# Kernel optimization log

Hardware: AMD Instinct MI355X
Metric: run time of the kernel (lower is better)

## Reference

```python
import jax, jax.numpy as jnp
import numpy as np

N = 100000
E = 1200000


def _gcn_norm(edge_index, num_nodes):
    # Add self-loops and compute symmetric normalization (PyG GCNConv default).
    row = jnp.concatenate([edge_index[0], jnp.arange(num_nodes, dtype=edge_index.dtype)])
    col = jnp.concatenate([edge_index[1], jnp.arange(num_nodes, dtype=edge_index.dtype)])
    deg = jax.ops.segment_sum(jnp.ones_like(col, dtype=jnp.float32), col, num_segments=num_nodes)
    dinv = jnp.where(deg > 0, jax.lax.rsqrt(jnp.maximum(deg, 1.0)), 0.0)
    norm = dinv[row] * dinv[col]  # [E+N]
    return row, col, norm


def _gcn_conv(x, W, b, row, col, norm, num_nodes):
    h = x @ W                      # [N, out] dense transform first (fewer bytes to gather)
    msg = h[row] * norm[:, None]   # gather + edge-wise scale
    out = jax.ops.segment_sum(msg, col, num_segments=num_nodes)  # scatter-add to targets
    return out + b


def setup_inputs() -> dict:
    key = jax.random.key(0)
    k1, k2, k3, k4 = jax.random.split(key, 4)
    x = jax.random.normal(k1, (N, 128), dtype=jnp.float32)
    edge_index = jax.random.randint(k2, (2, E), 0, N, dtype=jnp.int64)
    W1 = jax.random.normal(k3, (128, 256), dtype=jnp.float32) * (1.0 / np.sqrt(128))
    b1 = jnp.zeros((256,), dtype=jnp.float32)
    W2 = jax.random.normal(k4, (256, 40), dtype=jnp.float32) * (1.0 / np.sqrt(256))
    b2 = jnp.zeros((40,), dtype=jnp.float32)
    return {"x": x, "edge_index": edge_index, "W1": W1, "b1": b1, "W2": W2, "b2": b2}


def reference(x, edge_index, W1, b1, W2, b2):
    row, col, norm = _gcn_norm(edge_index, N)
    h = _gcn_conv(x, W1, b1, row, col, norm, N)
    h = jax.nn.relu(h)
    # dropout omitted: eval mode (training=False) is identity
    return _gcn_conv(h, W2, b2, row, col, norm, N)
```

## Files before the change

### kernel.cpp

```cpp
#include <hip/hip_runtime.h>
#include <hip/hip_bf16.h>

#define NN 100000
#define EE 1200000
#define F1 128
#define F2 256
#define F3 40
#define MROWS 64
#define NBUK ((NN + 255) / 256)
#define NBLK 256
#define CHUNK ((EE + NBLK - 1) / NBLK)
#define DCAP 4096
#define XB ((NN * 64 + 255) / 256)

typedef __bf16 bf16x8 __attribute__((ext_vector_type(8)));
typedef float  f32x4  __attribute__((ext_vector_type(4)));

__device__ __forceinline__ unsigned short f2bf(float f) {
    unsigned u = __float_as_uint(f);
    return (unsigned short)((u + 0x7fffu + ((u >> 16) & 1u)) >> 16);
}
__device__ __forceinline__ float bflo(unsigned v) { return __uint_as_float(v << 16); }
__device__ __forceinline__ float bfhi(unsigned v) { return __uint_as_float(v & 0xffff0000u); }

__global__ __launch_bounds__(256) void k_hist(const int* __restrict__ col,
                                              int* __restrict__ hist) {
    __shared__ int lh[NBUK];
    for (int i = threadIdx.x; i < NBUK; i += 256) lh[i] = 0;
    __syncthreads();
    int e0 = blockIdx.x * CHUNK;
    int e1 = min(e0 + CHUNK, EE);
    for (int e = e0 + threadIdx.x; e < e1; e += 256) {
        int c = col[e];
        if ((unsigned)c < (unsigned)NN) atomicAdd(&lh[c >> 8], 1);
    }
    __syncthreads();
    for (int i = threadIdx.x; i < NBUK; i += 256) hist[i * NBLK + blockIdx.x] = lh[i];
}

__global__ __launch_bounds__(256) void k_scanbin(int* __restrict__ hist,
                                                 int* __restrict__ bintot) {
    __shared__ int s[NBLK];
    int b = blockIdx.x;
    int v = hist[b * NBLK + threadIdx.x];
    s[threadIdx.x] = v;
    __syncthreads();
    int acc = v;
    for (int d = 1; d < NBLK; d <<= 1) {
        int add = (threadIdx.x >= d) ? s[threadIdx.x - d] : 0;
        __syncthreads();
        acc += add;
        s[threadIdx.x] = acc;
        __syncthreads();
    }
    hist[b * NBLK + threadIdx.x] = acc - v;
    if (threadIdx.x == NBLK - 1) bintot[b] = acc;
}

__global__ __launch_bounds__(512) void k_scanbase(const int* __restrict__ bintot,
                                                  int* __restrict__ binbase) {
    __shared__ int s[512];
    int v = (threadIdx.x < NBUK) ? bintot[threadIdx.x] : 0;
    s[threadIdx.x] = v;
    __syncthreads();
    int acc = v;
    for (int d = 1; d < 512; d <<= 1) {
        int add = (threadIdx.x >= d) ? s[threadIdx.x - d] : 0;
        __syncthreads();
        acc += add;
        s[threadIdx.x] = acc;
        __syncthreads();
    }
    if (threadIdx.x < NBUK) binbase[threadIdx.x] = acc - v;
    if (threadIdx.x == NBUK - 1) binbase[NBUK] = acc;
}

__global__ __launch_bounds__(256) void k_scat(const int* __restrict__ row,
                                              const int* __restrict__ col,
                                              const int* __restrict__ hist,
                                              const int* __restrict__ binbase,
                                              unsigned* __restrict__ rec) {
    __shared__ int lcur[NBUK];
    for (int i = threadIdx.x; i < NBUK; i += 256)
        lcur[i] = binbase[i] + hist[i * NBLK + blockIdx.x];
    __syncthreads();
    int e0 = blockIdx.x * CHUNK;
    int e1 = min(e0 + CHUNK, EE);
    for (int e = e0 + threadIdx.x; e < e1; e += 256) {
        int r = row[e], c = col[e];
        if ((unsigned)c < (unsigned)NN) {
            int pos = atomicAdd(&lcur[c >> 8], 1);
            rec[pos] = ((unsigned)r & 0xFFFFFFu) | ((unsigned)(c & 255) << 24);
        }
    }
}

__global__ __launch_bounds__(256) void k_csr(const int* __restrict__ binbase,
                                             const unsigned* __restrict__ rec,
                                             int* __restrict__ eidx,
                                             int* __restrict__ cnt,
                                             int* __restrict__ cursor,
                                             float* __restrict__ dinv) {
    __shared__ int lcnt[256];
    __shared__ int s[256];
    __shared__ int lcur[256];
    __shared__ int lde[DCAP];
    const int b = blockIdx.x;
    const int tid = threadIdx.x;
    lcnt[tid] = 0;
    __syncthreads();
    const int base = binbase[b];
    const int nb = min(binbase[b + 1] - base, DCAP);
    for (int j = tid; j < nb; j += 256) atomicAdd(&lcnt[rec[base + j] >> 24], 1);
    __syncthreads();
    int cv = lcnt[tid];
    s[tid] = cv;
    __syncthreads();
    int acc = cv;
    for (int d = 1; d < 256; d <<= 1) {
        int add = (tid >= d) ? s[tid - d] : 0;
        __syncthreads();
        acc += add;
        s[tid] = acc;
        __syncthreads();
    }
    int excl = acc - cv;
    lcur[tid] = excl;
    const int node = (b << 8) + tid;
    if (node < NN) {
        cnt[node] = cv;
        cursor[node] = base + excl + cv;
        dinv[node] = rsqrtf((float)(cv + 1));
    }
    __syncthreads();
    for (int j = tid; j < nb; j += 256) {
        unsigned v = rec[base + j];
        int pos = atomicAdd(&lcur[v >> 24], 1);
        lde[pos] = (int)(v & 0xFFFFFFu);
    }
    __syncthreads();
    for (int j = tid; j < nb; j += 256) eidx[base + j] = lde[j];
}

__global__ void k_prep(const float2* __restrict__ x, const float* __restrict__ dinv,
                       unsigned* __restrict__ xh,
                       const float* __restrict__ W1, const float* __restrict__ W2,
                       __hip_bfloat16* __restrict__ W1p, __hip_bfloat16* __restrict__ W2p) {
    if (blockIdx.x < XB) {
        int idx = blockIdx.x * 256 + threadIdx.x;
        if (idx < NN * 64) {
            float d = dinv[idx >> 6];
            float2 v = x[idx];
            xh[idx] = (unsigned)f2bf(v.x * d) | ((unsigned)f2bf(v.y * d) << 16);
        }
    } else {
        int idx = (blockIdx.x - XB) * 256 + threadIdx.x;
        if (idx < F1 * F2) {
            int k = idx / F2, col = idx - (idx / F2) * F2;
            int k8 = k >> 3, j = k & 7;
            W1p[((size_t)(k8 * F2 + col) << 3) + j] = __float2bfloat16(W1[(size_t)k * F2 + col]);
        } else if (idx < F1 * F2 + F2 * 48) {
            int i2 = idx - F1 * F2;
            int k = i2 / 48, col = i2 - (i2 / 48) * 48;
            int k8 = k >> 3, j = k & 7;
            float v = (col < F3) ? W2[(size_t)k * F3 + col] : 0.0f;
            W2p[((size_t)(k8 * 48 + col) << 3) + j] = __float2bfloat16(v);
        }
    }
}

__global__ __launch_bounds__(256) void k_agg1(const int* __restrict__ cursor,
                                              const int* __restrict__ cnt,
                                              const int* __restrict__ eidx,
                                              const float* __restrict__ dinv,
                                              const unsigned* __restrict__ xh,
                                              unsigned* __restrict__ agg) {
    int node = blockIdx.x * 4 + (threadIdx.x >> 6);
    int lane = threadIdx.x & 63;
    if (node >= NN) return;
    const int g = lane >> 4;
    const int l = lane & 15;
    float a0, a1, a2, a3, a4, a5, a6, a7;
    {
        uint4 v = {0u, 0u, 0u, 0u};
        if (g == 0) v = *(const uint4*)(xh + ((size_t)node << 6) + (l << 2));
        a0 = bflo(v.x); a1 = bfhi(v.x); a2 = bflo(v.y); a3 = bfhi(v.y);
        a4 = bflo(v.z); a5 = bfhi(v.z); a6 = bflo(v.w); a7 = bfhi(v.w);
    }
    int n = cnt[node];
    int s = cursor[node] - n;
    int k = 0;
    for (; k + 7 < n; k += 8) {
        int r0 = eidx[s + k + g];
        int r1 = eidx[s + k + 4 + g];
        uint4 v0 = *(const uint4*)(xh + ((size_t)r0 << 6) + (l << 2));
        uint4 v1 = *(const uint4*)(xh + ((size_t)r1 << 6) + (l << 2));
        a0 += bflo(v0.x); a1 += bfhi(v0.x); a2 += bflo(v0.y); a3 += bfhi(v0.y);
        a4 += bflo(v0.z); a5 += bfhi(v0.z); a6 += bflo(v0.w); a7 += bfhi(v0.w);
        a0 += bflo(v1.x); a1 += bfhi(v1.x); a2 += bflo(v1.y); a3 += bfhi(v1.y);
        a4 += bflo(v1.z); a5 += bfhi(v1.z); a6 += bflo(v1.w); a7 += bfhi(v1.w);
    }
    for (; k < n; k += 4) {
        if (k + g < n) {
            int r0 = eidx[s + k + g];
            uint4 v0 = *(const uint4*)(xh + ((size_t)r0 << 6) + (l << 2));
            a0 += bflo(v0.x); a1 += bfhi(v0.x); a2 += bflo(v0.y); a3 += bfhi(v0.y);
            a4 += bflo(v0.z); a5 += bfhi(v0.z); a6 += bflo(v0.w); a7 += bfhi(v0.w);
        }
    }
    a0 += __shfl_down(a0, 32, 64); a1 += __shfl_down(a1, 32, 64);
    a2 += __shfl_down(a2, 32, 64); a3 += __shfl_down(a3, 32, 64);
    a4 += __shfl_down(a4, 32, 64); a5 += __shfl_down(a5, 32, 64);
    a6 += __shfl_down(a6, 32, 64); a7 += __shfl_down(a7, 32, 64);
    a0 += __shfl_down(a0, 16, 64); a1 += __shfl_down(a1, 16, 64);
    a2 += __shfl_down(a2, 16, 64); a3 += __shfl_down(a3, 16, 64);
    a4 += __shfl_down(a4, 16, 64); a5 += __shfl_down(a5, 16, 64);
    a6 += __shfl_down(a6, 16, 64); a7 += __shfl_down(a7, 16, 64);
    if (g == 0) {
        float d = dinv[node];
        uint4 o;
        o.x = (unsigned)f2bf(a0 * d) | ((unsigned)f2bf(a1 * d) << 16);
        o.y = (unsigned)f2bf(a2 * d) | ((unsigned)f2bf(a3 * d) << 16);
        o.z = (unsigned)f2bf(a4 * d) | ((unsigned)f2bf(a5 * d) << 16);
        o.w = (unsigned)f2bf(a6 * d) | ((unsigned)f2bf(a7 * d) << 16);
        *(uint4*)(agg + ((size_t)node << 6) + (l << 2)) = o;
    }
}

__global__ __launch_bounds__(256) void k_gemm_mfma(
    const __hip_bfloat16* __restrict__ agg, const __hip_bfloat16* __restrict__ W1p,
    const float* __restrict__ b1, const __hip_bfloat16* __restrict__ W2p,
    const float* __restrict__ dinv, unsigned short* __restrict__ tg) {
    __shared__ __hip_bfloat16 h_s[MROWS][F2 + 8];
    const int i0   = blockIdx.x * MROWS;
    const int wave = threadIdx.x >> 6;
    const int lane = threadIdx.x & 63;
    const int m = lane & 15, q = lane >> 4;
    const int rowA = i0 + wave * 16 + m;

    f32x4 acc[16];
#pragma unroll
    for (int c = 0; c < 16; ++c) acc[c] = (f32x4){0.f, 0.f, 0.f, 0.f};

#pragma unroll
    for (int s = 0; s < 4; ++s) {
        bf16x8 a;
#pragma unroll
        for (int j = 0; j < 8; ++j) a[j] = (__bf16)0.0f;
        if (rowA < NN) a = *(const bf16x8*)(agg + (size_t)rowA * F1 + s * 32 + q * 8);
        const __hip_bfloat16* bp = W1p + ((size_t)(4 * s + q) * F2) * 8;
#pragma unroll
        for (int c = 0; c < 16; ++c) {
            bf16x8 b = *(const bf16x8*)(bp + ((size_t)(c * 16 + m) << 3));
            acc[c] = __builtin_amdgcn_mfma_f32_16x16x32_bf16(a, b, acc[c], 0, 0, 0);
        }
    }

#pragma unroll
    for (int c = 0; c < 16; ++c) {
        int col = c * 16 + m;
        float bj = b1[col];
#pragma unroll
        for (int r = 0; r < 4; ++r) {
            int lr = wave * 16 + q * 4 + r;
            h_s[lr][col] = __float2bfloat16(fmaxf(acc[c][r] + bj, 0.0f));
        }
    }
    __syncthreads();

    f32x4 acc2[3];
#pragma unroll
    for (int c = 0; c < 3; ++c) acc2[c] = (f32x4){0.f, 0.f, 0.f, 0.f};

#pragma unroll
    for (int s = 0; s < 8; ++s) {
        bf16x8 a = *(const bf16x8*)(&h_s[wave * 16 + m][s * 32 + q * 8]);
        const __hip_bfloat16* bp = W2p + ((size_t)(4 * s + q) * 48) * 8;
#pragma unroll
        for (int c = 0; c < 3; ++c) {
            bf16x8 b = *(const bf16x8*)(bp + ((size_t)(c * 16 + m) << 3));
            acc2[c] = __builtin_amdgcn_mfma_f32_16x16x32_bf16(a, b, acc2[c], 0, 0, 0);
        }
    }

#pragma unroll
    for (int c = 0; c < 3; ++c) {
        int col = c * 16 + m;
        if (col < F3) {
#pragma unroll
            for (int r = 0; r < 4; ++r) {
                int grow = i0 + wave * 16 + q * 4 + r;
                if (grow < NN)
                    tg[((size_t)grow << 6) + col] = f2bf(acc2[c][r] * dinv[grow]);
            }
        }
    }
}

__global__ __launch_bounds__(256) void k_agg2(const int* __restrict__ cursor,
                                              const int* __restrict__ cnt,
                                              const int* __restrict__ eidx,
                                              const float* __restrict__ dinv,
                                              const unsigned* __restrict__ tg32,
                                              const float* __restrict__ b2,
                                              float* __restrict__ out) {
    int node = blockIdx.x * 4 + (threadIdx.x >> 6);
    int lane = threadIdx.x & 63;
    if (node >= NN) return;
    const int g = lane / 20;
    const int l = lane - g * 20;
    const bool act = g < 3;
    float a0 = 0.f, a1 = 0.f;
    if (g == 0) {
        unsigned v = tg32[((size_t)node << 5) + l];
        a0 = bflo(v); a1 = bfhi(v);
    }
    int n = cnt[node];
    int s = cursor[node] - n;
    int k = 0;
    for (; k + 5 < n; k += 6) {
        unsigned v0 = 0u, v1 = 0u;
        if (act) {
            int r0 = eidx[s + k + g];
            int r1 = eidx[s + k + 3 + g];
            v0 = tg32[((size_t)r0 << 5) + l];
            v1 = tg32[((size_t)r1 << 5) + l];
        }
        a0 += bflo(v0); a1 += bfhi(v0);
        a0 += bflo(v1); a1 += bfhi(v1);
    }
    for (; k < n; k += 3) {
        if (act && (k + g) < n) {
            int r0 = eidx[s + k + g];
            unsigned v0 = tg32[((size_t)r0 << 5) + l];
            a0 += bflo(v0); a1 += bfhi(v0);
        }
    }
    float t0a = __shfl_down(a0, 20, 64), t0b = __shfl_down(a0, 40, 64);
    float t1a = __shfl_down(a1, 20, 64), t1b = __shfl_down(a1, 40, 64);
    if (lane < 20) {
        float d = dinv[node];
        float o0 = d * (a0 + t0a + t0b) + b2[2 * lane];
        float o1 = d * (a1 + t1a + t1b) + b2[2 * lane + 1];
        float2 o = {o0, o1};
        *(float2*)(out + (size_t)node * F3 + (lane << 1)) = o;
    }
}

extern "C" void kernel_launch(void* const* d_in, const int* in_sizes, int n_in,
                              void* d_out, int out_size, void* d_ws, size_t ws_size,
                              hipStream_t stream) {
    const float* x  = (const float*)d_in[0];
    const int*   ei = (const int*)d_in[1];
    const float* W1 = (const float*)d_in[2];
    const float* b1 = (const float*)d_in[3];
    const float* W2 = (const float*)d_in[4];
    const float* b2 = (const float*)d_in[5];
    float* out = (float*)d_out;

    const int* row = ei;
    const int* col = ei + EE;

    int* cnt     = (int*)d_ws;
    int* cursor  = cnt + NN;
    float* dinv  = (float*)(cursor + NN);
    int* hist    = (int*)(dinv + NN);
    int* bintot  = hist + NBUK * NBLK;
    int* binbase = bintot + NBUK;
    int* eidx    = binbase + (NBUK + 1) + 7;
    unsigned* xh  = (unsigned*)(eidx + EE);
    unsigned* agg = xh + (size_t)NN * 64;
    unsigned* rec = agg;
    unsigned short* tg = (unsigned short*)xh;
    __hip_bfloat16* W1p = (__hip_bfloat16*)(agg + (size_t)NN * 64);
    __hip_bfloat16* W2p = W1p + (size_t)F1 * F2;

    k_hist    <<<NBLK, 256, 0, stream>>>(col, hist);
    k_scanbin <<<NBUK, NBLK, 0, stream>>>(hist, bintot);
    k_scanbase<<<1, 512, 0, stream>>>(bintot, binbase);
    k_scat    <<<NBLK, 256, 0, stream>>>(row, col, hist, binbase, rec);
    k_csr     <<<NBUK, 256, 0, stream>>>(binbase, rec, eidx, cnt, cursor, dinv);

    k_prep<<<XB + (F1 * F2 + F2 * 48 + 255) / 256, 256, 0, stream>>>(
        (const float2*)x, dinv, xh, W1, W2, W1p, W2p);

    k_agg1<<<(NN + 3) / 4, 256, 0, stream>>>(cursor, cnt, eidx, dinv, xh, agg);
    k_gemm_mfma<<<(NN + MROWS - 1) / MROWS, 256, 0, stream>>>(
        (const __hip_bfloat16*)agg, W1p, b1, W2p, dinv, tg);
    k_agg2<<<(NN + 3) / 4, 256, 0, stream>>>(cursor, cnt, eidx, dinv,
                                             (const unsigned*)tg, b2, out);
}
```

Before: 302.3 us.

## Fuse x/weight prep into CSR kernel and vectorize histogram and scatter loads

Removes the separate k_prep kernel. Its weight-packing blocks become extra blocks of k_csr, and each CSR block now converts its own 256 nodes of x to dinv-scaled bf16 using dinv held in shared memory. The histogram and scatter kernels read col and row as int4, and the per-block histogram is stored block-major so each block writes and reads it contiguously. This saves a launch and a global reread of dinv, and widens edge loads. The cost is extra work per CSR block and strided access in the scan kernel.

After: 306.1 us. No clear change (+1.2%).

```diff
diff --git a/kernel.cpp b/kernel.cpp
--- a/kernel.cpp
+++ b/kernel.cpp
@@ -11,7 +11,7 @@
 #define NBLK 256
 #define CHUNK ((EE + NBLK - 1) / NBLK)
 #define DCAP 4096
-#define XB ((NN * 64 + 255) / 256)
+#define WB ((F1 * F2 + F2 * 48 + 255) / 256)
 
 typedef __bf16 bf16x8 __attribute__((ext_vector_type(8)));
 typedef float  f32x4  __attribute__((ext_vector_type(4)));
@@ -30,19 +30,22 @@
     __syncthreads();
     int e0 = blockIdx.x * CHUNK;
     int e1 = min(e0 + CHUNK, EE);
-    for (int e = e0 + threadIdx.x; e < e1; e += 256) {
-        int c = col[e];
-        if ((unsigned)c < (unsigned)NN) atomicAdd(&lh[c >> 8], 1);
-    }
-    __syncthreads();
-    for (int i = threadIdx.x; i < NBUK; i += 256) hist[i * NBLK + blockIdx.x] = lh[i];
+    for (int e = e0 + threadIdx.x * 4; e + 3 < e1; e += 1024) {
+        int4 c = *(const int4*)(col + e);
+        if ((unsigned)c.x < (unsigned)NN) atomicAdd(&lh[c.x >> 8], 1);
+        if ((unsigned)c.y < (unsigned)NN) atomicAdd(&lh[c.y >> 8], 1);
+        if ((unsigned)c.z < (unsigned)NN) atomicAdd(&lh[c.z >> 8], 1);
+        if ((unsigned)c.w < (unsigned)NN) atomicAdd(&lh[c.w >> 8], 1);
+    }
+    __syncthreads();
+    for (int i = threadIdx.x; i < NBUK; i += 256) hist[blockIdx.x * NBUK + i] = lh[i];
 }
 
 __global__ __launch_bounds__(256) void k_scanbin(int* __restrict__ hist,
                                                  int* __restrict__ bintot) {
     __shared__ int s[NBLK];
     int b = blockIdx.x;
-    int v = hist[b * NBLK + threadIdx.x];
+    int v = hist[threadIdx.x * NBUK + b];
     s[threadIdx.x] = v;
     __syncthreads();
     int acc = v;
@@ -53,7 +56,7 @@
         s[threadIdx.x] = acc;
         __syncthreads();
     }
-    hist[b * NBLK + threadIdx.x] = acc - v;
+    hist[threadIdx.x * NBUK + b] = acc - v;
     if (threadIdx.x == NBLK - 1) bintot[b] = acc;
 }
 
@@ -82,15 +85,28 @@
                                               unsigned* __restrict__ rec) {
     __shared__ int lcur[NBUK];
     for (int i = threadIdx.x; i < NBUK; i += 256)
-        lcur[i] = binbase[i] + hist[i * NBLK + blockIdx.x];
+        lcur[i] = binbase[i] + hist[blockIdx.x * NBUK + i];
     __syncthreads();
     int e0 = blockIdx.x * CHUNK;
     int e1 = min(e0 + CHUNK, EE);
-    for (int e = e0 + threadIdx.x; e < e1; e += 256) {
-        int r = row[e], c = col[e];
-        if ((unsigned)c < (unsigned)NN) {
-            int pos = atomicAdd(&lcur[c >> 8], 1);
-            rec[pos] = ((unsigned)r & 0xFFFFFFu) | ((unsigned)(c & 255) << 24);
+    for (int e = e0 + threadIdx.x * 4; e + 3 < e1; e += 1024) {
+        int4 r = *(const int4*)(row + e);
+        int4 c = *(const int4*)(col + e);
+        if ((unsigned)c.x < (unsigned)NN) {
+            int p = atomicAdd(&lcur[c.x >> 8], 1);
+            rec[p] = ((unsigned)r.x & 0xFFFFFFu) | ((unsigned)(c.x & 255) << 24);
+        }
+        if ((unsigned)c.y < (unsigned)NN) {
+            int p = atomicAdd(&lcur[c.y >> 8], 1);
+            rec[p] = ((unsigned)r.y & 0xFFFFFFu) | ((unsigned)(c.y & 255) << 24);
+        }
+        if ((unsigned)c.z < (unsigned)NN) {
+            int p = atomicAdd(&lcur[c.z >> 8], 1);
+            rec[p] = ((unsigned)r.z & 0xFFFFFFu) | ((unsigned)(c.z & 255) << 24);
+        }
+        if ((unsigned)c.w < (unsigned)NN) {
+            int p = atomicAdd(&lcur[c.w >> 8], 1);
+            rec[p] = ((unsigned)r.w & 0xFFFFFFu) | ((unsigned)(c.w & 255) << 24);
         }
     }
 }
@@ -100,10 +116,32 @@
                                              int* __restrict__ eidx,
                                              int* __restrict__ cnt,
                                              int* __restrict__ cursor,
-                                             float* __restrict__ dinv) {
+                                             float* __restrict__ dinv,
+                                             const float4* __restrict__ x4,
+                                             unsigned* __restrict__ xh,
+                                             const float* __restrict__ W1,
+                                             const float* __restrict__ W2,
+                                             __hip_bfloat16* __restrict__ W1p,
+                                             __hip_bfloat16* __restrict__ W2p) {
+    if (blockIdx.x >= NBUK) {
+        int idx = (blockIdx.x - NBUK) * 256 + threadIdx.x;
+        if (idx < F1 * F2) {
+            int k = idx / F2, colw = idx - (idx / F2) * F2;
+            int k8 = k >> 3, j = k & 7;
+            W1p[((size_t)(k8 * F2 + colw) << 3) + j] = __float2bfloat16(W1[(size_t)k * F2 + colw]);
+        } else if (idx < F1 * F2 + F2 * 48) {
+            int i2 = idx - F1 * F2;
+            int k = i2 / 48, colw = i2 - (i2 / 48) * 48;
+            int k8 = k >> 3, j = k & 7;
+            float v = (colw < F3) ? W2[(size_t)k * F3 + colw] : 0.0f;
+            W2p[((size_t)(k8 * 48 + colw) << 3) + j] = __float2bfloat16(v);
+        }
+        return;
+    }
     __shared__ int lcnt[256];
     __shared__ int s[256];
     __shared__ int lcur[256];
+    __shared__ float sdinv[256];
     __shared__ int lde[DCAP];
     const int b = blockIdx.x;
     const int tid = threadIdx.x;
@@ -127,10 +165,12 @@
     int excl = acc - cv;
     lcur[tid] = excl;
     const int node = (b << 8) + tid;
+    float dv = rsqrtf((float)(cv + 1));
+    sdinv[tid] = dv;
     if (node < NN) {
         cnt[node] = cv;
         cursor[node] = base + excl + cv;
-        dinv[node] = rsqrtf((float)(cv + 1));
+        dinv[node] = dv;
     }
     __syncthreads();
     for (int j = tid; j < nb; j += 256) {
@@ -140,31 +180,16 @@
     }
     __syncthreads();
     for (int j = tid; j < nb; j += 256) eidx[base + j] = lde[j];
-}
-
-__global__ void k_prep(const float2* __restrict__ x, const float* __restrict__ dinv,
-                       unsigned* __restrict__ xh,
-                       const float* __restrict__ W1, const float* __restrict__ W2,
-                       __hip_bfloat16* __restrict__ W1p, __hip_bfloat16* __restrict__ W2p) {
-    if (blockIdx.x < XB) {
-        int idx = blockIdx.x * 256 + threadIdx.x;
-        if (idx < NN * 64) {
-            float d = dinv[idx >> 6];
-            float2 v = x[idx];
-            xh[idx] = (unsigned)f2bf(v.x * d) | ((unsigned)f2bf(v.y * d) << 16);
-        }
-    } else {
-        int idx = (blockIdx.x - XB) * 256 + threadIdx.x;
-        if (idx < F1 * F2) {
-            int k = idx / F2, col = idx - (idx / F2) * F2;
-            int k8 = k >> 3, j = k & 7;
-            W1p[((size_t)(k8 * F2 + col) << 3) + j] = __float2bfloat16(W1[(size_t)k * F2 + col]);
-        } else if (idx < F1 * F2 + F2 * 48) {
-            int i2 = idx - F1 * F2;
-            int k = i2 / 48, col = i2 - (i2 / 48) * 48;
-            int k8 = k >> 3, j = k & 7;
-            float v = (col < F3) ? W2[(size_t)k * F3 + col] : 0.0f;
-            W2p[((size_t)(k8 * 48 + col) << 3) + j] = __float2bfloat16(v);
+    for (int j = tid; j < 256 * 32; j += 256) {
+        int nl = j >> 5;
+        int gn = (b << 8) + nl;
+        if (gn < NN) {
+            float d = sdinv[nl];
+            float4 v = x4[(size_t)gn * 32 + (j & 31)];
+            uint2 o;
+            o.x = (unsigned)f2bf(v.x * d) | ((unsigned)f2bf(v.y * d) << 16);
+            o.y = (unsigned)f2bf(v.z * d) | ((unsigned)f2bf(v.w * d) << 16);
+            *(uint2*)(xh + ((size_t)gn << 6) + ((j & 31) << 1)) = o;
         }
     }
 }
@@ -365,7 +390,7 @@
     int* cursor  = cnt + NN;
     float* dinv  = (float*)(cursor + NN);
     int* hist    = (int*)(dinv + NN);
-    int* bintot  = hist + NBUK * NBLK;
+    int* bintot  = hist + NBLK * NBUK;
     int* binbase = bintot + NBUK;
     int* eidx    = binbase + (NBUK + 1) + 7;
     unsigned* xh  = (unsigned*)(eidx + EE);
@@ -379,10 +404,8 @@
     k_scanbin <<<NBUK, NBLK, 0, stream>>>(hist, bintot);
     k_scanbase<<<1, 512, 0, stream>>>(bintot, binbase);
     k_scat    <<<NBLK, 256, 0, stream>>>(row, col, hist, binbase, rec);
-    k_csr     <<<NBUK, 256, 0, stream>>>(binbase, rec, eidx, cnt, cursor, dinv);
-
-    k_prep<<<XB + (F1 * F2 + F2 * 48 + 255) / 256, 256, 0, stream>>>(
-        (const float2*)x, dinv, xh, W1, W2, W1p, W2p);
+    k_csr     <<<NBUK + WB, 256, 0, stream>>>(binbase, rec, eidx, cnt, cursor, dinv,
+                                              (const float4*)x, xh, W1, W2, W1p, W2p);
 
     k_agg1<<<(NN + 3) / 4, 256, 0, stream>>>(cursor, cnt, eidx, dinv, xh, agg);
     k_gemm_mfma<<<(NN + MROWS - 1) / MROWS, 256, 0, stream>>>(
```
